# Performance work log

Hardware: AMD Instinct MI355X
Metric: run time of the kernel (lower is better)

Reference implementation:

```python
import jax, jax.numpy as jnp
import numpy as np

B, F, S, D, H = 32, 4096, 8, 512, 2048
N_ITERS = 3
EPS = 1e-8
SCALE = D ** -0.5
LN_EPS = 1e-5  # torch LayerNorm default


def setup_inputs() -> dict:
    key = jax.random.key(0)
    ks = jax.random.split(key, 16)
    w = lambda k, shp: (jax.random.normal(k, shp) * 0.02).astype(jnp.float32)
    d = {
        "slots": jax.random.normal(ks[0], (B, S, D), dtype=jnp.float32),
        "features": jax.random.normal(ks[1], (B, F, D), dtype=jnp.float32),
        # projection weights, stored (in, out) so y = x @ W
        "w_k": w(ks[2], (D, D)),
        "w_v": w(ks[3], (D, D)),
        "w_q": w(ks[4], (D, D)),
        # layer norms
        "ln_feat_w": jnp.ones(D, jnp.float32), "ln_feat_b": jnp.zeros(D, jnp.float32),
        "ln_slot_w": jnp.ones(D, jnp.float32), "ln_slot_b": jnp.zeros(D, jnp.float32),
        # GRUCell (torch layout: gates [r, z, n] stacked on dim0 of [3D, D])
        "gru_w_ih": w(ks[5], (3 * D, D)),
        "gru_w_hh": w(ks[6], (3 * D, D)),
        "gru_b_ih": jnp.zeros(3 * D, jnp.float32),
        "gru_b_hh": jnp.zeros(3 * D, jnp.float32),
        # residual MLP: LN -> Linear(D,H) -> relu -> Linear(H,D)
        "ln_mlp_w": jnp.ones(D, jnp.float32), "ln_mlp_b": jnp.zeros(D, jnp.float32),
        "mlp_w1": w(ks[7], (D, H)), "mlp_b1": jnp.zeros(H, jnp.float32),
        "mlp_w2": w(ks[8], (H, D)), "mlp_b2": jnp.zeros(D, jnp.float32),
    }
    return d


def _ln(x, w, b):
    m = jnp.mean(x, axis=-1, keepdims=True)
    v = jnp.mean(jnp.square(x - m), axis=-1, keepdims=True)
    return (x - m) * jax.lax.rsqrt(v + LN_EPS) * w + b


def _gru_cell(x, h, w_ih, w_hh, b_ih, b_hh):
    # torch.nn.GRUCell semantics; x,h: [..., D]
    gi = x @ w_ih.T + b_ih
    gh = h @ w_hh.T + b_hh
    i_r, i_z, i_n = jnp.split(gi, 3, axis=-1)
    h_r, h_z, h_n = jnp.split(gh, 3, axis=-1)
    r = jax.nn.sigmoid(i_r + h_r)
    z = jax.nn.sigmoid(i_z + h_z)
    n = jnp.tanh(i_n + r * h_n)
    return (1.0 - z) * n + z * h


def reference(slots, features, w_k, w_v, w_q, ln_feat_w, ln_feat_b,
              ln_slot_w, ln_slot_b, gru_w_ih, gru_w_hh, gru_b_ih, gru_b_hh,
              ln_mlp_w, ln_mlp_b, mlp_w1, mlp_b1, mlp_w2, mlp_b2):
    f = _ln(features, ln_feat_w, ln_feat_b)          # [B,F,D]
    keys = f @ w_k                                    # [B,F,D]
    values = f @ w_v                                  # [B,F,D]
    pre_norm_attn = None
    for _ in range(N_ITERS):
        s_n = _ln(slots, ln_slot_w, ln_slot_b)        # [B,S,D]
        q = s_n @ w_q                                 # [B,S,D]
        dots = jnp.einsum('bsd,bfd->bsf', q, keys) * SCALE
        pre_norm_attn = jax.nn.softmax(dots, axis=1)  # softmax over SLOTS
        attn = pre_norm_attn + EPS
        attn = attn / jnp.sum(attn, axis=-1, keepdims=True)
        updates = jnp.einsum('bsf,bfd->bsd', attn, values)
        slots = _gru_cell(updates, s_n, gru_w_ih, gru_w_hh, gru_b_ih, gru_b_hh)
        # residual MLP with initial LayerNorm
        h = _ln(slots, ln_mlp_w, ln_mlp_b)
        h = jax.nn.relu(h @ mlp_w1 + mlp_b1) @ mlp_w2 + mlp_b2
        slots = slots + h
    return slots, pre_norm_attn
```

## Files before the change

kernel.cpp:

```cpp
#include <hip/hip_runtime.h>
#include <hip/hip_bf16.h>
#include <stdint.h>

typedef __hip_bfloat16 bf16;
typedef unsigned short ushort_t;

#define B_ 32
#define F_ 4096
#define S_ 8
#define D_ 512
#define H_ 2048
#define LN_EPS 1e-5f
#define EPS_ 1e-8f
#define SCALE_ 0.044194173824159216f

__device__ __forceinline__ float b2f(ushort_t u){
  union { uint32_t i; float f; } c; c.i = ((uint32_t)u) << 16; return c.f;
}
__device__ __forceinline__ float4 ld4f(const float* p){ return *(const float4*)p; }
__device__ __forceinline__ float4 ld4h(const ushort_t* p){
  ushort4 u = *(const ushort4*)p;
  return make_float4(b2f(u.x), b2f(u.y), b2f(u.z), b2f(u.w));
}
__device__ __forceinline__ float allsum64(float v){
  #pragma unroll
  for (int o = 1; o < 64; o <<= 1) v += __shfl_xor(v, o, 64);
  return v;
}
__device__ __forceinline__ float blockSum256(float v, float* sh){
  v = allsum64(v);
  int wid = threadIdx.x >> 6, lane = threadIdx.x & 63;
  __syncthreads();
  if (lane == 0) sh[wid] = v;
  __syncthreads();
  return sh[0] + sh[1] + sh[2] + sh[3];
}
__device__ __forceinline__ float dynld(const void* p, int i, bool f32){
  return f32 ? ((const float*)p)[i] : b2f(((const ushort_t*)p)[i]);
}

__global__ void detect_dtype(const uint32_t* __restrict__ w, int* __restrict__ flag){
  __shared__ int sh;
  if (threadIdx.x == 0) sh = 0;
  __syncthreads();
  int c = 0;
  for (int i = threadIdx.x; i < 4096; i += 256){
    uint32_t e = (w[i] >> 7) & 0xFF;
    if (e == 0 || e >= 0xBF) c++;
  }
  atomicAdd(&sh, c);
  __syncthreads();
  if (threadIdx.x == 0) *flag = (sh >= 100) ? 1 : 0;
}

template<int TRANS_B, int A_DYN, int B_DYN, int A_CMB>
__global__ __launch_bounds__(256) void gemm64(
    const void* __restrict__ A, const void* __restrict__ B,
    const void* __restrict__ Abias, float* __restrict__ C,
    int M, int N, int K, int kLen, size_t aPart, const int* __restrict__ flag)
{
  const bool f32 = (*flag != 0);
  const bool aF = A_DYN ? f32 : true;
  const bool bF = B_DYN ? f32 : true;
  __shared__ float As[16][68];
  __shared__ float Bs[16][68];
  const int tid = threadIdx.x;
  const int m0 = blockIdx.x * 64, n0 = blockIdx.y * 64;
  const int kBeg = blockIdx.z * kLen;
  const int tm = (tid & 15) * 4, tn = (tid >> 4) * 4;
  const int ar = tid >> 2;
  const int ac = (tid & 3) * 4;
  const int br = tid >> 4;
  const int bc = (tid & 15) * 4;
  float acc[4][4] = {};

  for (int kc = kBeg; kc < kBeg + kLen; kc += 16){
    size_t aidx = (size_t)(m0 + ar) * K + kc + ac;
    float4 a4;
    if (A_CMB){
      const float* Af = (const float*)A;
      float4 s0 = ld4f(Af + aidx);
      float4 s1 = ld4f(Af + aPart + aidx);
      float4 s2 = ld4f(Af + 2 * aPart + aidx);
      float4 s3 = ld4f(Af + 3 * aPart + aidx);
      float bx0 = dynld(Abias, kc + ac + 0, f32);
      float bx1 = dynld(Abias, kc + ac + 1, f32);
      float bx2 = dynld(Abias, kc + ac + 2, f32);
      float bx3 = dynld(Abias, kc + ac + 3, f32);
      a4.x = fmaxf(s0.x + s1.x + s2.x + s3.x + bx0, 0.0f);
      a4.y = fmaxf(s0.y + s1.y + s2.y + s3.y + bx1, 0.0f);
      a4.z = fmaxf(s0.z + s1.z + s2.z + s3.z + bx2, 0.0f);
      a4.w = fmaxf(s0.w + s1.w + s2.w + s3.w + bx3, 0.0f);
    } else {
      a4 = aF ? ld4f((const float*)A + aidx) : ld4h((const ushort_t*)A + aidx);
    }
    As[ac+0][ar] = a4.x; As[ac+1][ar] = a4.y; As[ac+2][ar] = a4.z; As[ac+3][ar] = a4.w;
    if (!TRANS_B){
      size_t bidx = (size_t)(kc + br) * N + n0 + bc;
      float4 b4 = bF ? ld4f((const float*)B + bidx) : ld4h((const ushort_t*)B + bidx);
      Bs[br][bc+0] = b4.x; Bs[br][bc+1] = b4.y; Bs[br][bc+2] = b4.z; Bs[br][bc+3] = b4.w;
    } else {
      size_t bidx = (size_t)(n0 + ar) * K + kc + ac;
      float4 b4 = bF ? ld4f((const float*)B + bidx) : ld4h((const ushort_t*)B + bidx);
      Bs[ac+0][ar] = b4.x; Bs[ac+1][ar] = b4.y; Bs[ac+2][ar] = b4.z; Bs[ac+3][ar] = b4.w;
    }
    __syncthreads();
    #pragma unroll
    for (int k = 0; k < 16; k++){
      float av[4], bv[4];
      #pragma unroll
      for (int i = 0; i < 4; i++) av[i] = As[k][tm + i];
      #pragma unroll
      for (int j = 0; j < 4; j++) bv[j] = Bs[k][tn + j];
      #pragma unroll
      for (int i = 0; i < 4; i++)
        #pragma unroll
        for (int j = 0; j < 4; j++) acc[i][j] += av[i] * bv[j];
    }
    __syncthreads();
  }
  #pragma unroll
  for (int i = 0; i < 4; i++)
    #pragma unroll
    for (int j = 0; j < 4; j++)
      C[((size_t)blockIdx.z * M + m0 + tm + i) * N + n0 + tn + j] = acc[i][j];
}

__global__ __launch_bounds__(256) void combine4(
    const float* __restrict__ in, float* __restrict__ out, int sz)
{
  int i = blockIdx.x * 256 + threadIdx.x;
  out[i] = in[i] + in[sz + i] + in[2 * sz + i] + in[3 * sz + i];
}

__global__ __launch_bounds__(256) void gemm_gigh(
    const float* __restrict__ Ud, const float* __restrict__ Wvih,
    const float* __restrict__ s_n, const void* __restrict__ w_hh,
    float* __restrict__ gip, float* __restrict__ ghp,
    const int* __restrict__ flag)
{
  const bool f32 = (*flag != 0);
  const bool doGh = blockIdx.z >= 4;
  const int kz = blockIdx.z & 3;
  __shared__ float As[16][68];
  __shared__ float Bs[16][68];
  const int tid = threadIdx.x;
  const int m0 = blockIdx.x * 64, n0 = blockIdx.y * 64;
  const int kBeg = kz * 128;
  const int tm = (tid & 15) * 4, tn = (tid >> 4) * 4;
  const int ar = tid >> 2;
  const int ac = (tid & 3) * 4;
  const int br = tid >> 4;
  const int bc = (tid & 15) * 4;
  const float* A = doGh ? s_n : Ud;
  float acc[4][4] = {};

  for (int kc = kBeg; kc < kBeg + 128; kc += 16){
    float4 a4 = ld4f(A + (size_t)(m0 + ar) * 512 + kc + ac);
    As[ac+0][ar] = a4.x; As[ac+1][ar] = a4.y; As[ac+2][ar] = a4.z; As[ac+3][ar] = a4.w;
    if (!doGh){
      float4 b4 = ld4f(Wvih + (size_t)(kc + br) * 1536 + n0 + bc);
      Bs[br][bc+0] = b4.x; Bs[br][bc+1] = b4.y; Bs[br][bc+2] = b4.z; Bs[br][bc+3] = b4.w;
    } else {
      size_t bidx = (size_t)(n0 + ar) * 512 + kc + ac;
      float4 b4 = f32 ? ld4f((const float*)w_hh + bidx)
                      : ld4h((const ushort_t*)w_hh + bidx);
      Bs[ac+0][ar] = b4.x; Bs[ac+1][ar] = b4.y; Bs[ac+2][ar] = b4.z; Bs[ac+3][ar] = b4.w;
    }
    __syncthreads();
    #pragma unroll
    for (int k = 0; k < 16; k++){
      float av[4], bv[4];
      #pragma unroll
      for (int i = 0; i < 4; i++) av[i] = As[k][tm + i];
      #pragma unroll
      for (int j = 0; j < 4; j++) bv[j] = Bs[k][tn + j];
      #pragma unroll
      for (int i = 0; i < 4; i++)
        #pragma unroll
        for (int j = 0; j < 4; j++) acc[i][j] += av[i] * bv[j];
    }
    __syncthreads();
  }
  float* C = (doGh ? ghp : gip) + (size_t)kz * 256 * 1536;
  #pragma unroll
  for (int i = 0; i < 4; i++)
    #pragma unroll
    for (int j = 0; j < 4; j++)
      C[(size_t)(m0 + tm + i) * 1536 + n0 + tn + j] = acc[i][j];
}

template<int F32>
__device__ __forceinline__ void bp_rows(
    const void* __restrict__ features, size_t base,
    const float (&lw)[8], const float (&lb)[8], const float (&qkr)[8][8],
    float (&U)[8][8], float (&racc)[8], float (*pbuf)[128], int wid, int lane)
{
  const float* fbf = (const float*)features + base;
  const ushort_t* fbh = (const ushort_t*)features + base;
  float4 nf0 = {}, nf1 = {}; uint4 nh = {};
  if (F32){ nf0 = *(const float4*)fbf; nf1 = *(const float4*)(fbf + 4); }
  else    { nh  = *(const uint4*)fbh; }

  for (int r = 0; r < 32; r++){
    float x[8];
    if (F32){
      float4 c0 = nf0, c1 = nf1;
      if (r < 31){
        nf0 = *(const float4*)(fbf + (size_t)(r + 1) * D_);
        nf1 = *(const float4*)(fbf + (size_t)(r + 1) * D_ + 4);
      }
      x[0]=c0.x; x[1]=c0.y; x[2]=c0.z; x[3]=c0.w;
      x[4]=c1.x; x[5]=c1.y; x[6]=c1.z; x[7]=c1.w;
    } else {
      uint4 cx = nh;
      if (r < 31) nh = *(const uint4*)(fbh + (size_t)(r + 1) * D_);
      x[0]=b2f(cx.x & 0xffff); x[1]=b2f(cx.x >> 16);
      x[2]=b2f(cx.y & 0xffff); x[3]=b2f(cx.y >> 16);
      x[4]=b2f(cx.z & 0xffff); x[5]=b2f(cx.z >> 16);
      x[6]=b2f(cx.w & 0xffff); x[7]=b2f(cx.w >> 16);
    }
    float sum = 0.0f;
    #pragma unroll
    for (int j = 0; j < 8; j++) sum += x[j];
    float mean = allsum64(sum) * (1.0f / 512.0f);
    float var = 0.0f;
    #pragma unroll
    for (int j = 0; j < 8; j++){ x[j] -= mean; var += x[j] * x[j]; }
    var = allsum64(var) * (1.0f / 512.0f);
    float rstd = 1.0f / sqrtf(var + LN_EPS);
    float y[8];
    #pragma unroll
    for (int j = 0; j < 8; j++) y[j] = x[j] * rstd * lw[j] + lb[j];

    float dt[8];
    #pragma unroll
    for (int s = 0; s < 8; s++){
      float t = 0.0f;
      #pragma unroll
      for (int j = 0; j < 8; j++) t += qkr[s][j] * y[j];
      dt[s] = allsum64(t) * SCALE_;
    }
    float mx = dt[0];
    #pragma unroll
    for (int s = 1; s < 8; s++) mx = fmaxf(mx, dt[s]);
    float p[8]; float den = 0.0f;
    #pragma unroll
    for (int s = 0; s < 8; s++){ p[s] = __expf(dt[s] - mx); den += p[s]; }
    float inv = 1.0f / den;
    #pragma unroll
    for (int s = 0; s < 8; s++) p[s] *= inv;
    #pragma unroll
    for (int s = 0; s < 8; s++) if (lane == s) pbuf[s][wid * 32 + r] = p[s];
    #pragma unroll
    for (int s = 0; s < 8; s++){
      float pe = p[s] + EPS_;
      racc[s] += pe;
      #pragma unroll
      for (int j = 0; j < 8; j++) U[s][j] += pe * y[j];
    }
  }
}

__global__ __launch_bounds__(256, 2) void big_pass(
    const void* __restrict__ features, const float* __restrict__ qkp,
    const void* __restrict__ lnw, const void* __restrict__ lnb,
    void* __restrict__ d_out_base, float* __restrict__ Upart,
    float* __restrict__ Rpart, const int* __restrict__ flag)
{
  const bool f32rt = (*flag != 0);
  __shared__ float Ubuf[4][2 * D_];
  __shared__ float pbuf[S_][128];
  __shared__ float Rbuf[4][S_];
  const int b = blockIdx.y;
  const int tid = threadIdx.x;
  const int wid = tid >> 6, lane = tid & 63;
  const int fblock = blockIdx.x * 128;
  const int f0 = fblock + wid * 32;

  float lw[8], lb[8];
  #pragma unroll
  for (int j = 0; j < 8; j++){
    int d = 8 * lane + j;
    lw[j] = dynld(lnw, d, f32rt);
    lb[j] = dynld(lnb, d, f32rt);
  }
  float qkr[8][8];
  #pragma unroll
  for (int s = 0; s < 8; s++){
    const float* qp = qkp + (size_t)(b * S_ + s) * D_ + 8 * lane;
    float4 q0 = ld4f(qp);
    float4 q1 = ld4f(qp + 4);
    #pragma unroll
    for (int p = 1; p < 4; p++){
      const float* qq = qp + (size_t)p * 131072;
      float4 t0 = ld4f(qq), t1 = ld4f(qq + 4);
      q0.x += t0.x; q0.y += t0.y; q0.z += t0.z; q0.w += t0.w;
      q1.x += t1.x; q1.y += t1.y; q1.z += t1.z; q1.w += t1.w;
    }
    qkr[s][0]=q0.x; qkr[s][1]=q0.y; qkr[s][2]=q0.z; qkr[s][3]=q0.w;
    qkr[s][4]=q1.x; qkr[s][5]=q1.y; qkr[s][6]=q1.z; qkr[s][7]=q1.w;
  }
  float U[8][8] = {};
  float racc[8] = {0,0,0,0,0,0,0,0};
  const size_t base = ((size_t)b * F_ + f0) * D_ + 8 * lane;

  if (f32rt) bp_rows<1>(features, base, lw, lb, qkr, U, racc, pbuf, wid, lane);
  else       bp_rows<0>(features, base, lw, lb, qkr, U, racc, pbuf, wid, lane);

  #pragma unroll
  for (int s = 0; s < 8; s++) if (lane == s) Rbuf[wid][s] = racc[s];
  __syncthreads();
  #pragma unroll
  for (int e2 = 0; e2 < 4; e2++){
    int e = tid + e2 * 256;
    int s = e >> 7, c = e & 127;
    size_t oi = 131072 + ((size_t)(b * S_ + s)) * F_ + fblock + c;
    float pv = pbuf[s][c];
    if (f32rt) ((float*)d_out_base)[oi] = pv;
    else       ((bf16*)d_out_base)[oi] = __float2bfloat16(pv);
  }
  if (tid < 8)
    Rpart[((size_t)b * 32 + blockIdx.x) * 8 + tid] =
        Rbuf[0][tid] + Rbuf[1][tid] + Rbuf[2][tid] + Rbuf[3][tid];
  float* up = Upart + ((size_t)b * 32 + blockIdx.x) * (S_ * D_);
  #pragma unroll
  for (int g = 0; g < 4; g++){
    #pragma unroll
    for (int h = 0; h < 2; h++){
      float* ub = &Ubuf[wid][h * D_ + 8 * lane];
      *(float4*)ub     = make_float4(U[2*g+h][0], U[2*g+h][1], U[2*g+h][2], U[2*g+h][3]);
      *(float4*)(ub+4) = make_float4(U[2*g+h][4], U[2*g+h][5], U[2*g+h][6], U[2*g+h][7]);
    }
    __syncthreads();
    for (int e = tid; e < 2 * D_; e += 256)
      up[g * 2 * D_ + e] = Ubuf[0][e] + Ubuf[1][e] + Ubuf[2][e] + Ubuf[3][e];
    if (g < 3) __syncthreads();
  }
}

__global__ __launch_bounds__(256) void reduce_updates(
    const float* __restrict__ Upart, const float* __restrict__ Rpart,
    float* __restrict__ Ud)
{
  __shared__ float rinv;
  int bs = blockIdx.x;
  int b = bs >> 3, s = bs & 7;
  int t = threadIdx.x;
  if (t == 0){
    float r = 0.0f;
    for (int w = 0; w < 32; w++) r += Rpart[((size_t)(b * 32 + w)) * 8 + s];
    rinv = 1.0f / r;
  }
  __syncthreads();
  const float* up = Upart + ((size_t)b * 32 * 8 + s) * 512;
  float ri = rinv;
  #pragma unroll
  for (int u = 0; u < 2; u++){
    int e = t + u * 256;
    float acc = 0.0f;
    for (int w = 0; w < 32; w++) acc += up[(size_t)w * 4096 + e];
    Ud[((size_t)(b * S_ + s)) * D_ + e] = acc * ri;
  }
}

__global__ __launch_bounds__(256) void ln_rows(
    const float* __restrict__ x, const void* __restrict__ w,
    const void* __restrict__ b, float* __restrict__ y, const int* __restrict__ flag)
{
  const bool f32 = (*flag != 0);
  __shared__ float sh[4];
  int row = blockIdx.x, t = threadIdx.x;
  const float* xr = x + (size_t)row * D_;
  float v0 = xr[t], v1 = xr[t + 256];
  float mean = blockSum256(v0 + v1, sh) * (1.0f / 512.0f);
  float d0 = v0 - mean, d1 = v1 - mean;
  float var = blockSum256(d0 * d0 + d1 * d1, sh) * (1.0f / 512.0f);
  float rstd = 1.0f / sqrtf(var + LN_EPS);
  float w0 = dynld(w, t, f32),       w1 = dynld(w, t + 256, f32);
  float b0 = dynld(b, t, f32),       b1 = dynld(b, t + 256, f32);
  y[(size_t)row * D_ + t]       = d0 * rstd * w0 + b0;
  y[(size_t)row * D_ + t + 256] = d1 * rstd * w1 + b1;
}

__global__ __launch_bounds__(256) void gru_combine(
    const float* __restrict__ gip, const float* __restrict__ ghp,
    const void* __restrict__ b_ih, const void* __restrict__ b_hh,
    const float* __restrict__ sn, const void* __restrict__ lw,
    const void* __restrict__ lb, float* __restrict__ snew,
    float* __restrict__ lnm, const int* __restrict__ flag)
{
  const bool f32 = (*flag != 0);
  __shared__ float sh[4];
  int row = blockIdx.x, t = threadIdx.x;
  const float* snr = sn + (size_t)row * D_;
  float v[2];
  #pragma unroll
  for (int u = 0; u < 2; u++){
    int d = t + u * 256;
    float ir = 0, iz = 0, in_ = 0, hr = 0, hz = 0, hn = 0;
    #pragma unroll
    for (int p = 0; p < 4; p++){
      const float* gp = gip + (size_t)p * 393216 + (size_t)row * 1536;
      const float* hp = ghp + (size_t)p * 393216 + (size_t)row * 1536;
      ir  += gp[d]; iz += gp[512 + d]; in_ += gp[1024 + d];
      hr  += hp[d]; hz += hp[512 + d]; hn  += hp[1024 + d];
    }
    ir  += dynld(b_ih, d, f32);
    iz  += dynld(b_ih, 512 + d, f32);
    in_ += dynld(b_ih, 1024 + d, f32);
    hr  += dynld(b_hh, d, f32);
    hz  += dynld(b_hh, 512 + d, f32);
    hn  += dynld(b_hh, 1024 + d, f32);
    float rg = 1.0f / (1.0f + __expf(-(ir + hr)));
    float zg = 1.0f / (1.0f + __expf(-(iz + hz)));
    float a  = in_ + rg * hn;
    float e2 = __expf(2.0f * a);
    float ng = 1.0f - 2.0f / (e2 + 1.0f);
    float h  = snr[d];
    v[u] = (1.0f - zg) * ng + zg * h;
    snew[(size_t)row * D_ + d] = v[u];
  }
  float mean = blockSum256(v[0] + v[1], sh) * (1.0f / 512.0f);
  float d0 = v[0] - mean, d1 = v[1] - mean;
  float var = blockSum256(d0 * d0 + d1 * d1, sh) * (1.0f / 512.0f);
  float rstd = 1.0f / sqrtf(var + LN_EPS);
  float w0 = dynld(lw, t, f32),       w1 = dynld(lw, t + 256, f32);
  float b0 = dynld(lb, t, f32),       b1 = dynld(lb, t + 256, f32);
  lnm[(size_t)row * D_ + t]       = d0 * rstd * w0 + b0;
  lnm[(size_t)row * D_ + t + 256] = d1 * rstd * w1 + b1;
}

template<int FINAL>
__global__ __launch_bounds__(256) void combine_ln(
    const float* __restrict__ snew, const float* __restrict__ h2p,
    const void* __restrict__ b2, const void* __restrict__ lnw,
    const void* __restrict__ lnb, float* __restrict__ s_n,
    void* __restrict__ out, const int* __restrict__ flag)
{
  const bool f32 = (*flag != 0);
  __shared__ float sh[4];
  int row = blockIdx.x, t = threadIdx.x;
  float v[2];
  #pragma unroll
  for (int u = 0; u < 2; u++){
    int d = t + u * 256;
    size_t idx = (size_t)row * D_ + d;
    float acc = snew[idx];
    #pragma unroll
    for (int p = 0; p < 8; p++) acc += h2p[(size_t)p * 131072 + idx];
    acc += dynld(b2, d, f32);
    v[u] = acc;
    if (FINAL){
      if (f32) ((float*)out)[idx] = acc;
      else     ((bf16*)out)[idx] = __float2bfloat16(acc);
    }
  }
  if (!FINAL){
    float mean = blockSum256(v[0] + v[1], sh) * (1.0f / 512.0f);
    float d0 = v[0] - mean, d1 = v[1] - mean;
    float var = blockSum256(d0 * d0 + d1 * d1, sh) * (1.0f / 512.0f);
    float rstd = 1.0f / sqrtf(var + LN_EPS);
    float w0 = dynld(lnw, t, f32),       w1 = dynld(lnw, t + 256, f32);
    float b0 = dynld(lnb, t, f32),       b1 = dynld(lnb, t + 256, f32);
    s_n[(size_t)row * D_ + t]       = d0 * rstd * w0 + b0;
    s_n[(size_t)row * D_ + t + 256] = d1 * rstd * w1 + b1;
  }
}

__global__ __launch_bounds__(256) void cast_in(const void* __restrict__ in,
                                               float* __restrict__ out,
                                               const int* __restrict__ flag){
  const bool f32 = (*flag != 0);
  int i = blockIdx.x * 256 + threadIdx.x;
  out[i] = f32 ? ((const float*)in)[i] : b2f(((const ushort_t*)in)[i]);
}

extern "C" void kernel_launch(void* const* d_in, const int* in_sizes, int n_in,
                              void* d_out, int out_size, void* d_ws, size_t ws_size,
                              hipStream_t stream)
{
  const void* in_slots  = d_in[0];
  const void* features  = d_in[1];
  const void* w_k   = d_in[2];
  const void* w_v   = d_in[3];
  const void* w_q   = d_in[4];
  const void* ln_feat_w = d_in[5];
  const void* ln_feat_b = d_in[6];
  const void* ln_slot_w = d_in[7];
  const void* ln_slot_b = d_in[8];
  const void* w_ih  = d_in[9];
  const void* w_hh  = d_in[10];
  const void* b_ih  = d_in[11];
  const void* b_hh  = d_in[12];
  const void* ln_mlp_w = d_in[13];
  const void* ln_mlp_b = d_in[14];
  const void* mlp_w1 = d_in[15];
  const void* mlp_b1 = d_in[16];
  const void* mlp_w2 = d_in[17];
  const void* mlp_b2 = d_in[18];

  float* W     = (float*)d_ws;
  int*   flag  = (int*)d_ws;
  float* Wqk   = W + 64;
  float* slots = Wqk   + 262144;
  float* s_n   = slots + 131072;
  float* qkp   = s_n   + 131072;
  float* Ud    = qkp   + 524288;
  float* Rpart = Ud    + 131072;
  float* Upart = Rpart + 8192;
  float* gip   = Upart + 4194304;
  float* ghp   = gip   + 1572864;
  float* lnm   = ghp   + 1572864;
  float* snew  = lnm   + 131072;
  float* h1p   = snew  + 131072;
  float* h2p   = h1p   + 2097152;
  float* Wqkp  = h2p   + 1048576;
  float* Wvih  = Wqkp  + 1048576;

  detect_dtype<<<1, 256, 0, stream>>>((const uint32_t*)features, flag);
  cast_in<<<512, 256, 0, stream>>>(in_slots, slots, flag);
  gemm64<1, 1, 1, 0><<<dim3(8, 8, 4), 256, 0, stream>>>(
      w_q, w_k, nullptr, Wqkp, 512, 512, 512, 128, 0, flag);
  combine4<<<1024, 256, 0, stream>>>(Wqkp, Wqk, 262144);
  gemm64<1, 1, 1, 0><<<dim3(8, 24, 1), 256, 0, stream>>>(
      w_v, w_ih, nullptr, Wvih, 512, 1536, 512, 512, 0, flag);
  ln_rows<<<256, 256, 0, stream>>>(slots, ln_slot_w, ln_slot_b, s_n, flag);

  for (int it = 0; it < 3; ++it){
    gemm64<0, 0, 0, 0><<<dim3(4, 8, 4), 256, 0, stream>>>(
        s_n, Wqk, nullptr, qkp, 256, 512, 512, 128, 0, flag);
    big_pass<<<dim3(32, 32), 256, 0, stream>>>(
        features, qkp, ln_feat_w, ln_feat_b, d_out, Upart, Rpart, flag);
    reduce_updates<<<256, 256, 0, stream>>>(Upart, Rpart, Ud);
    gemm_gigh<<<dim3(4, 24, 8), 256, 0, stream>>>(
        Ud, Wvih, s_n, w_hh, gip, ghp, flag);
    gru_combine<<<256, 256, 0, stream>>>(gip, ghp, b_ih, b_hh, s_n,
                                         ln_mlp_w, ln_mlp_b, snew, lnm, flag);
    gemm64<0, 0, 1, 0><<<dim3(4, 32, 4), 256, 0, stream>>>(
        lnm, mlp_w1, nullptr, h1p, 256, 2048, 512, 128, 0, flag);
    gemm64<0, 0, 1, 1><<<dim3(4, 8, 8), 256, 0, stream>>>(
        h1p, mlp_w2, mlp_b1, h2p, 256, 512, 2048, 256, 524288, flag);
    if (it < 2)
      combine_ln<0><<<256, 256, 0, stream>>>(snew, h2p, mlp_b2, ln_slot_w,
                                             ln_slot_b, s_n, d_out, flag);
    else
      combine_ln<1><<<256, 256, 0, stream>>>(snew, h2p, mlp_b2, ln_slot_w,
                                             ln_slot_b, s_n, d_out, flag);
  }
}
```

Before: 1.052 ms.

## Fold feature LayerNorm algebraically into attention and precompute row stats once

Computes per-row mean and rstd of features once before the loop. Each iteration folds the LN weight and bias into the query vector and applies mean/rstd as scalar corrections, so the attention logits come straight from raw features. The update accumulation likewise runs on raw features with rstd-scaled weights, and the mean/bias correction is applied in the reduction. This removes the per-iteration LN and wave-wide shuffle reductions. The cost is that features are read twice per iteration, with a one-thread-per-row access pattern that is poorly coalesced, plus slightly different numerics from the one-pass variance.

```diff
diff --git a/kernel.cpp b/kernel.cpp
--- a/kernel.cpp
+++ b/kernel.cpp
@@ -190,177 +190,244 @@
       C[(size_t)(m0 + tm + i) * 1536 + n0 + tn + j] = acc[i][j];
 }
 
+__global__ __launch_bounds__(256, 2) void ln_stats(
+    const void* __restrict__ features, float* __restrict__ meanb,
+    float* __restrict__ rstdb, const int* __restrict__ flag)
+{
+  const bool f32 = (*flag != 0);
+  const int b = blockIdx.y;
+  const int tid = threadIdx.x, wid = tid >> 6, lane = tid & 63;
+  const int f0 = blockIdx.x * 128 + wid * 32;
+  const size_t base = ((size_t)b * F_ + f0) * D_ + 8 * lane;
+  if (f32){
+    const float* fp = (const float*)features + base;
+    for (int r = 0; r < 32; r++){
+      float4 c0 = ld4f(fp + (size_t)r * D_);
+      float4 c1 = ld4f(fp + (size_t)r * D_ + 4);
+      float s1 = c0.x+c0.y+c0.z+c0.w + c1.x+c1.y+c1.z+c1.w;
+      float s2 = c0.x*c0.x+c0.y*c0.y+c0.z*c0.z+c0.w*c0.w
+               + c1.x*c1.x+c1.y*c1.y+c1.z*c1.z+c1.w*c1.w;
+      s1 = allsum64(s1); s2 = allsum64(s2);
+      if (lane == 0){
+        float mean = s1 * (1.0f/512.0f);
+        float var = fmaxf(s2 * (1.0f/512.0f) - mean*mean, 0.0f);
+        meanb[b * F_ + f0 + r] = mean;
+        rstdb[b * F_ + f0 + r] = 1.0f / sqrtf(var + LN_EPS);
+      }
+    }
+  } else {
+    const ushort_t* fp = (const ushort_t*)features + base;
+    for (int r = 0; r < 32; r++){
+      uint4 u = *(const uint4*)(fp + (size_t)r * D_);
+      float x0=b2f(u.x&0xffff), x1=b2f(u.x>>16), x2=b2f(u.y&0xffff), x3=b2f(u.y>>16);
+      float x4=b2f(u.z&0xffff), x5=b2f(u.z>>16), x6=b2f(u.w&0xffff), x7=b2f(u.w>>16);
+      float s1 = x0+x1+x2+x3+x4+x5+x6+x7;
+      float s2 = x0*x0+x1*x1+x2*x2+x3*x3+x4*x4+x5*x5+x6*x6+x7*x7;
+      s1 = allsum64(s1); s2 = allsum64(s2);
+      if (lane == 0){
+        float mean = s1 * (1.0f/512.0f);
+        float var = fmaxf(s2 * (1.0f/512.0f) - mean*mean, 0.0f);
+        meanb[b * F_ + f0 + r] = mean;
+        rstdb[b * F_ + f0 + r] = 1.0f / sqrtf(var + LN_EPS);
+      }
+    }
+  }
+}
+
+__global__ __launch_bounds__(256) void qk_prep(
+    const float* __restrict__ qkp, const void* __restrict__ lnw,
+    const void* __restrict__ lnb, float* __restrict__ gbuf,
+    float* __restrict__ gsb, float* __restrict__ qbb,
+    const int* __restrict__ flag)
+{
+  const bool f32 = (*flag != 0);
+  __shared__ float sh[4];
+  const int b = blockIdx.x, t = threadIdx.x;
+  #pragma unroll
+  for (int s = 0; s < 8; s++){
+    float gsum = 0.0f, qbsum = 0.0f;
+    #pragma unroll
+    for (int u = 0; u < 2; u++){
+      int d = t + u * 256;
+      size_t idx = (size_t)(b * 8 + s) * 512 + d;
+      float q = qkp[idx] + qkp[131072 + idx] + qkp[262144 + idx] + qkp[393216 + idx];
+      float lwv = dynld(lnw, d, f32), lbv = dynld(lnb, d, f32);
+      float g = SCALE_ * q * lwv;
+      gbuf[(size_t)b * 4096 + s * 512 + d] = g;
+      gsum += g;
+      qbsum += SCALE_ * q * lbv;
+    }
+    float gs = blockSum256(gsum, sh);
+    float qb = blockSum256(qbsum, sh);
+    if (t == 0){ gsb[b * 8 + s] = gs; qbb[b * 8 + s] = qb; }
+  }
+}
+
 template<int F32>
-__device__ __forceinline__ void bp_rows(
-    const void* __restrict__ features, size_t base,
-    const float (&lw)[8], const float (&lb)[8], const float (&qkr)[8][8],
-    float (&U)[8][8], float (&racc)[8], float (*pbuf)[128], int wid, int lane)
-{
-  const float* fbf = (const float*)features + base;
-  const ushort_t* fbh = (const ushort_t*)features + base;
-  float4 nf0 = {}, nf1 = {}; uint4 nh = {};
-  if (F32){ nf0 = *(const float4*)fbf; nf1 = *(const float4*)(fbf + 4); }
-  else    { nh  = *(const uint4*)fbh; }
-
-  for (int r = 0; r < 32; r++){
-    float x[8];
-    if (F32){
-      float4 c0 = nf0, c1 = nf1;
-      if (r < 31){
-        nf0 = *(const float4*)(fbf + (size_t)(r + 1) * D_);
-        nf1 = *(const float4*)(fbf + (size_t)(r + 1) * D_ + 4);
+__device__ __forceinline__ void bp2_phase1(
+    const void* __restrict__ features, const float* __restrict__ gb,
+    size_t rowbase, float (&acc)[8])
+{
+  if (F32){
+    const float* fp = (const float*)features + rowbase;
+    for (int c = 0; c < 128; c++){
+      float4 xv = ld4f(fp + c * 4);
+      #pragma unroll
+      for (int s = 0; s < 8; s++){
+        float4 g4 = ld4f(gb + s * 512 + c * 4);
+        acc[s] += g4.x*xv.x + g4.y*xv.y + g4.z*xv.z + g4.w*xv.w;
       }
-      x[0]=c0.x; x[1]=c0.y; x[2]=c0.z; x[3]=c0.w;
-      x[4]=c1.x; x[5]=c1.y; x[6]=c1.z; x[7]=c1.w;
-    } else {
-      uint4 cx = nh;
-      if (r < 31) nh = *(const uint4*)(fbh + (size_t)(r + 1) * D_);
-      x[0]=b2f(cx.x & 0xffff); x[1]=b2f(cx.x >> 16);
-      x[2]=b2f(cx.y & 0xffff); x[3]=b2f(cx.y >> 16);
-      x[4]=b2f(cx.z & 0xffff); x[5]=b2f(cx.z >> 16);
-      x[6]=b2f(cx.w & 0xffff); x[7]=b2f(cx.w >> 16);
-    }
-    float sum = 0.0f;
-    #pragma unroll
-    for (int j = 0; j < 8; j++) sum += x[j];
-    float mean = allsum64(sum) * (1.0f / 512.0f);
-    float var = 0.0f;
-    #pragma unroll
-    for (int j = 0; j < 8; j++){ x[j] -= mean; var += x[j] * x[j]; }
-    var = allsum64(var) * (1.0f / 512.0f);
-    float rstd = 1.0f / sqrtf(var + LN_EPS);
-    float y[8];
-    #pragma unroll
-    for (int j = 0; j < 8; j++) y[j] = x[j] * rstd * lw[j] + lb[j];
-
-    float dt[8];
-    #pragma unroll
-    for (int s = 0; s < 8; s++){
-      float t = 0.0f;
-      #pragma unroll
-      for (int j = 0; j < 8; j++) t += qkr[s][j] * y[j];
-      dt[s] = allsum64(t) * SCALE_;
-    }
-    float mx = dt[0];
-    #pragma unroll
-    for (int s = 1; s < 8; s++) mx = fmaxf(mx, dt[s]);
-    float p[8]; float den = 0.0f;
-    #pragma unroll
-    for (int s = 0; s < 8; s++){ p[s] = __expf(dt[s] - mx); den += p[s]; }
-    float inv = 1.0f / den;
-    #pragma unroll
-    for (int s = 0; s < 8; s++) p[s] *= inv;
-    #pragma unroll
-    for (int s = 0; s < 8; s++) if (lane == s) pbuf[s][wid * 32 + r] = p[s];
-    #pragma unroll
-    for (int s = 0; s < 8; s++){
-      float pe = p[s] + EPS_;
-      racc[s] += pe;
-      #pragma unroll
-      for (int j = 0; j < 8; j++) U[s][j] += pe * y[j];
-    }
-  }
-}
-
-__global__ __launch_bounds__(256, 2) void big_pass(
-    const void* __restrict__ features, const float* __restrict__ qkp,
-    const void* __restrict__ lnw, const void* __restrict__ lnb,
-    void* __restrict__ d_out_base, float* __restrict__ Upart,
-    float* __restrict__ Rpart, const int* __restrict__ flag)
-{
-  const bool f32rt = (*flag != 0);
-  __shared__ float Ubuf[4][2 * D_];
-  __shared__ float pbuf[S_][128];
-  __shared__ float Rbuf[4][S_];
-  const int b = blockIdx.y;
-  const int tid = threadIdx.x;
-  const int wid = tid >> 6, lane = tid & 63;
-  const int fblock = blockIdx.x * 128;
-  const int f0 = fblock + wid * 32;
-
-  float lw[8], lb[8];
-  #pragma unroll
-  for (int j = 0; j < 8; j++){
-    int d = 8 * lane + j;
-    lw[j] = dynld(lnw, d, f32rt);
-    lb[j] = dynld(lnb, d, f32rt);
-  }
-  float qkr[8][8];
+    }
+  } else {
+    const ushort_t* fp = (const ushort_t*)features + rowbase;
+    for (int c = 0; c < 64; c++){
+      uint4 u = *(const uint4*)(fp + c * 8);
+      float x0=b2f(u.x&0xffff), x1=b2f(u.x>>16), x2=b2f(u.y&0xffff), x3=b2f(u.y>>16);
+      float x4=b2f(u.z&0xffff), x5=b2f(u.z>>16), x6=b2f(u.w&0xffff), x7=b2f(u.w>>16);
+      #pragma unroll
+      for (int s = 0; s < 8; s++){
+        float4 ga = ld4f(gb + s * 512 + c * 8);
+        float4 gc = ld4f(gb + s * 512 + c * 8 + 4);
+        acc[s] += ga.x*x0 + ga.y*x1 + ga.z*x2 + ga.w*x3
+                + gc.x*x4 + gc.y*x5 + gc.z*x6 + gc.w*x7;
+      }
+    }
+  }
+}
+
+template<int F32>
+__device__ __forceinline__ void bp2_phase2(
+    const void* __restrict__ features, size_t tb, const float* __restrict__ Pl,
+    int s2, int dq, float (&a1)[16])
+{
+  if (F32){
+    const float* fp = (const float*)features + tb + dq * 16;
+    for (int r = 0; r < 256; r++){
+      float pw = Pl[s2 * 256 + r];
+      const float* rp = fp + (size_t)r * D_;
+      float4 x0 = ld4f(rp), x1 = ld4f(rp + 4), x2 = ld4f(rp + 8), x3 = ld4f(rp + 12);
+      a1[0]  += pw*x0.x; a1[1]  += pw*x0.y; a1[2]  += pw*x0.z; a1[3]  += pw*x0.w;
+      a1[4]  += pw*x1.x; a1[5]  += pw*x1.y; a1[6]  += pw*x1.z; a1[7]  += pw*x1.w;
+      a1[8]  += pw*x2.x; a1[9]  += pw*x2.y; a1[10] += pw*x2.z; a1[11] += pw*x2.w;
+      a1[12] += pw*x3.x; a1[13] += pw*x3.y; a1[14] += pw*x3.z; a1[15] += pw*x3.w;
+    }
+  } else {
+    const ushort_t* fp = (const ushort_t*)features + tb + dq * 16;
+    for (int r = 0; r < 256; r++){
+      float pw = Pl[s2 * 256 + r];
+      const ushort_t* rp = fp + (size_t)r * D_;
+      uint4 u0 = *(const uint4*)rp;
+      uint4 u1 = *(const uint4*)(rp + 8);
+      a1[0]  += pw*b2f(u0.x&0xffff); a1[1]  += pw*b2f(u0.x>>16);
+      a1[2]  += pw*b2f(u0.y&0xffff); a1[3]  += pw*b2f(u0.y>>16);
+      a1[4]  += pw*b2f(u0.z&0xffff); a1[5]  += pw*b2f(u0.z>>16);
+      a1[6]  += pw*b2f(u0.w&0xffff); a1[7]  += pw*b2f(u0.w>>16);
+      a1[8]  += pw*b2f(u1.x&0xffff); a1[9]  += pw*b2f(u1.x>>16);
+      a1[10] += pw*b2f(u1.y&0xffff); a1[11] += pw*b2f(u1.y>>16);
+      a1[12] += pw*b2f(u1.z&0xffff); a1[13] += pw*b2f(u1.z>>16);
+      a1[14] += pw*b2f(u1.w&0xffff); a1[15] += pw*b2f(u1.w>>16);
+    }
+  }
+}
+
+__global__ __launch_bounds__(256, 2) void big_pass2(
+    const void* __restrict__ features, const float* __restrict__ gbuf,
+    const float* __restrict__ gsb, const float* __restrict__ qbb,
+    const float* __restrict__ meanb, const float* __restrict__ rstdb,
+    void* __restrict__ d_out_base, float* __restrict__ A1p,
+    float* __restrict__ A2p, float* __restrict__ A3p,
+    const int* __restrict__ flag)
+{
+  const bool f32 = (*flag != 0);
+  __shared__ float Pl[8 * 256];
+  __shared__ float sh[4];
+  const int b = blockIdx.y, fg = blockIdx.x, t = threadIdx.x;
+  const int f0 = fg * 256;
+  const int row = f0 + t;
+  const float* gb = gbuf + (size_t)b * 4096;
+  const float mean = meanb[b * F_ + row];
+  const float rstd = rstdb[b * F_ + row];
+
+  float acc[8] = {};
+  const size_t rowbase = ((size_t)b * F_ + row) * D_;
+  if (f32) bp2_phase1<1>(features, gb, rowbase, acc);
+  else     bp2_phase1<0>(features, gb, rowbase, acc);
+
+  float dt[8];
+  #pragma unroll
+  for (int s = 0; s < 8; s++)
+    dt[s] = rstd * (acc[s] - mean * gsb[b * 8 + s]) + qbb[b * 8 + s];
+  float mx = dt[0];
+  #pragma unroll
+  for (int s = 1; s < 8; s++) mx = fmaxf(mx, dt[s]);
+  float p[8]; float den = 0.0f;
+  #pragma unroll
+  for (int s = 0; s < 8; s++){ p[s] = __expf(dt[s] - mx); den += p[s]; }
+  float inv = 1.0f / den;
+  #pragma unroll
+  for (int s = 0; s < 8; s++) p[s] *= inv;
   #pragma unroll
   for (int s = 0; s < 8; s++){
-    const float* qp = qkp + (size_t)(b * S_ + s) * D_ + 8 * lane;
-    float4 q0 = ld4f(qp);
-    float4 q1 = ld4f(qp + 4);
-    #pragma unroll
-    for (int p = 1; p < 4; p++){
-      const float* qq = qp + (size_t)p * 131072;
-      float4 t0 = ld4f(qq), t1 = ld4f(qq + 4);
-      q0.x += t0.x; q0.y += t0.y; q0.z += t0.z; q0.w += t0.w;
-      q1.x += t1.x; q1.y += t1.y; q1.z += t1.z; q1.w += t1.w;
-    }
-    qkr[s][0]=q0.x; qkr[s][1]=q0.y; qkr[s][2]=q0.z; qkr[s][3]=q0.w;
-    qkr[s][4]=q1.x; qkr[s][5]=q1.y; qkr[s][6]=q1.z; qkr[s][7]=q1.w;
-  }
-  float U[8][8] = {};
-  float racc[8] = {0,0,0,0,0,0,0,0};
-  const size_t base = ((size_t)b * F_ + f0) * D_ + 8 * lane;
-
-  if (f32rt) bp_rows<1>(features, base, lw, lb, qkr, U, racc, pbuf, wid, lane);
-  else       bp_rows<0>(features, base, lw, lb, qkr, U, racc, pbuf, wid, lane);
-
-  #pragma unroll
-  for (int s = 0; s < 8; s++) if (lane == s) Rbuf[wid][s] = racc[s];
+    size_t oi = 131072 + ((size_t)(b * 8 + s)) * F_ + row;
+    if (f32) ((float*)d_out_base)[oi] = p[s];
+    else     ((bf16*)d_out_base)[oi] = __float2bfloat16(p[s]);
+  }
+  float a2[8], a3[8];
+  #pragma unroll
+  for (int s = 0; s < 8; s++){
+    float pe = p[s] + EPS_;
+    Pl[s * 256 + t] = pe * rstd;
+    a2[s] = pe * rstd * mean;
+    a3[s] = pe;
+  }
+  const int bidx = b * 16 + fg;
+  #pragma unroll
+  for (int s = 0; s < 8; s++){
+    float v2 = blockSum256(a2[s], sh);
+    float v3 = blockSum256(a3[s], sh);
+    if (t == s){ A2p[bidx * 8 + s] = v2; A3p[bidx * 8 + s] = v3; }
+  }
   __syncthreads();
-  #pragma unroll
-  for (int e2 = 0; e2 < 4; e2++){
-    int e = tid + e2 * 256;
-    int s = e >> 7, c = e & 127;
-    size_t oi = 131072 + ((size_t)(b * S_ + s)) * F_ + fblock + c;
-    float pv = pbuf[s][c];
-    if (f32rt) ((float*)d_out_base)[oi] = pv;
-    else       ((bf16*)d_out_base)[oi] = __float2bfloat16(pv);
-  }
-  if (tid < 8)
-    Rpart[((size_t)b * 32 + blockIdx.x) * 8 + tid] =
-        Rbuf[0][tid] + Rbuf[1][tid] + Rbuf[2][tid] + Rbuf[3][tid];
-  float* up = Upart + ((size_t)b * 32 + blockIdx.x) * (S_ * D_);
-  #pragma unroll
-  for (int g = 0; g < 4; g++){
-    #pragma unroll
-    for (int h = 0; h < 2; h++){
-      float* ub = &Ubuf[wid][h * D_ + 8 * lane];
-      *(float4*)ub     = make_float4(U[2*g+h][0], U[2*g+h][1], U[2*g+h][2], U[2*g+h][3]);
-      *(float4*)(ub+4) = make_float4(U[2*g+h][4], U[2*g+h][5], U[2*g+h][6], U[2*g+h][7]);
-    }
-    __syncthreads();
-    for (int e = tid; e < 2 * D_; e += 256)
-      up[g * 2 * D_ + e] = Ubuf[0][e] + Ubuf[1][e] + Ubuf[2][e] + Ubuf[3][e];
-    if (g < 3) __syncthreads();
-  }
-}
-
-__global__ __launch_bounds__(256) void reduce_updates(
-    const float* __restrict__ Upart, const float* __restrict__ Rpart,
-    float* __restrict__ Ud)
-{
-  __shared__ float rinv;
-  int bs = blockIdx.x;
-  int b = bs >> 3, s = bs & 7;
-  int t = threadIdx.x;
+  const int s2 = t >> 5, dq = t & 31;
+  float a1[16] = {};
+  const size_t tb = ((size_t)b * F_ + f0) * D_;
+  if (f32) bp2_phase2<1>(features, tb, Pl, s2, dq, a1);
+  else     bp2_phase2<0>(features, tb, Pl, s2, dq, a1);
+  float* up = A1p + ((size_t)bidx) * 4096 + s2 * 512 + dq * 16;
+  #pragma unroll
+  for (int j = 0; j < 4; j++)
+    *(float4*)(up + j * 4) = make_float4(a1[4*j], a1[4*j+1], a1[4*j+2], a1[4*j+3]);
+}
+
+__global__ __launch_bounds__(256) void reduce_updates2(
+    const float* __restrict__ A1p, const float* __restrict__ A2p,
+    const float* __restrict__ A3p, const void* __restrict__ lnw,
+    const void* __restrict__ lnb, float* __restrict__ Ud,
+    const int* __restrict__ flag)
+{
+  const bool f32 = (*flag != 0);
+  __shared__ float sc[2];
+  const int blk = blockIdx.x;
+  const int b = blk >> 3, s = blk & 7;
+  const int t = threadIdx.x;
   if (t == 0){
-    float r = 0.0f;
-    for (int w = 0; w < 32; w++) r += Rpart[((size_t)(b * 32 + w)) * 8 + s];
-    rinv = 1.0f / r;
+    float R = 0.0f, C = 0.0f;
+    for (int fg = 0; fg < 16; fg++){
+      R += A3p[(b * 16 + fg) * 8 + s];
+      C += A2p[(b * 16 + fg) * 8 + s];
+    }
+    sc[0] = 1.0f / R; sc[1] = C;
   }
   __syncthreads();
-  const float* up = Upart + ((size_t)b * 32 * 8 + s) * 512;
-  float ri = rinv;
+  const float rinv = sc[0], C = sc[1];
   #pragma unroll
   for (int u = 0; u < 2; u++){
-    int e = t + u * 256;
-    float acc = 0.0f;
-    for (int w = 0; w < 32; w++) acc += up[(size_t)w * 4096 + e];
-    Ud[((size_t)(b * S_ + s)) * D_ + e] = acc * ri;
+    int d = t + u * 256;
+    float a = 0.0f;
+    for (int fg = 0; fg < 16; fg++)
+      a += A1p[((size_t)(b * 16 + fg)) * 4096 + s * 512 + d];
+    float lwv = dynld(lnw, d, f32), lbv = dynld(lnb, d, f32);
+    Ud[((size_t)(b * 8 + s)) * 512 + d] = lwv * (a - C) * rinv + lbv;
   }
 }
 
@@ -507,9 +574,15 @@
   float* s_n   = slots + 131072;
   float* qkp   = s_n   + 131072;
   float* Ud    = qkp   + 524288;
-  float* Rpart = Ud    + 131072;
-  float* Upart = Rpart + 8192;
-  float* gip   = Upart + 4194304;
+  float* meanb = Ud    + 131072;
+  float* rstdb = meanb + 131072;
+  float* gbuf  = rstdb + 131072;
+  float* gsb   = gbuf  + 131072;
+  float* qbb   = gsb   + 256;
+  float* A1p   = qbb   + 256;
+  float* A2p   = A1p   + 2097152;
+  float* A3p   = A2p   + 4096;
+  float* gip   = A3p   + 4096;
   float* ghp   = gip   + 1572864;
   float* lnm   = ghp   + 1572864;
   float* snew  = lnm   + 131072;
@@ -525,14 +598,18 @@
   combine4<<<1024, 256, 0, stream>>>(Wqkp, Wqk, 262144);
   gemm64<1, 1, 1, 0><<<dim3(8, 24, 1), 256, 0, stream>>>(
       w_v, w_ih, nullptr, Wvih, 512, 1536, 512, 512, 0, flag);
+  ln_stats<<<dim3(32, 32), 256, 0, stream>>>(features, meanb, rstdb, flag);
   ln_rows<<<256, 256, 0, stream>>>(slots, ln_slot_w, ln_slot_b, s_n, flag);
 
   for (int it = 0; it < 3; ++it){
     gemm64<0, 0, 0, 0><<<dim3(4, 8, 4), 256, 0, stream>>>(
         s_n, Wqk, nullptr, qkp, 256, 512, 512, 128, 0, flag);
-    big_pass<<<dim3(32, 32), 256, 0, stream>>>(
-        features, qkp, ln_feat_w, ln_feat_b, d_out, Upart, Rpart, flag);
-    reduce_updates<<<256, 256, 0, stream>>>(Upart, Rpart, Ud);
+    qk_prep<<<32, 256, 0, stream>>>(qkp, ln_feat_w, ln_feat_b,
+                                    gbuf, gsb, qbb, flag);
+    big_pass2<<<dim3(16, 32), 256, 0, stream>>>(
+        features, gbuf, gsb, qbb, meanb, rstdb, d_out, A1p, A2p, A3p, flag);
+    reduce_updates2<<<256, 256, 0, stream>>>(A1p, A2p, A3p, ln_feat_w,
+                                             ln_feat_b, Ud, flag);
     gemm_gigh<<<dim3(4, 24, 8), 256, 0, stream>>>(
         Ud, Wvih, s_n, w_hh, gip, ghp, flag);
     gru_combine<<<256, 256, 0, stream>>>(gip, ghp, b_ih, b_hh, s_n,
```

Result: slower. 1.397 ms (+32.8%).
